# Optimization experiments

Measured on AMD Instinct MI355X. Metric: run time of the kernel, lower is better.

The kernel has to match this reference:

```python
import jax, jax.numpy as jnp
import numpy as np

B, S, H, Q, K = 16, 4096, 1024, 1024, 2048


def setup_inputs() -> dict:
    key = jax.random.key(0)
    k0, k1, k2, k3, k4, k5 = jax.random.split(key, 6)
    return {
        "mask": jax.random.randint(k0, (B, 1, S), 0, 2, dtype=jnp.int32),
        "query": jax.random.normal(k1, (B, 1, Q), dtype=jnp.float32),
        "proj_key": jax.random.normal(k2, (B, S, H), dtype=jnp.float32),
        "value": jax.random.normal(k3, (B, S, K), dtype=jnp.float32),
        "Wq": jax.random.normal(k4, (H, Q), dtype=jnp.float32) * 0.02,
        "w_energy": jax.random.normal(k5, (H,), dtype=jnp.float32) * 0.02,
    }


def reference(mask, query, proj_key, value, Wq, w_energy):
    # query_layer: [B,1,Q] @ Wq^T -> [B,1,H]
    q = jnp.einsum("btq,hq->bth", query, Wq)
    # energy_layer(tanh(q + proj_key)): broadcast add over seq, dot with w_energy -> [B,S]
    scores = jnp.einsum("bsh,h->bs", jnp.tanh(q + proj_key), w_energy)
    scores = scores[:, None, :]  # [B,1,S]
    scores = jnp.where(mask == 0, -jnp.inf, scores)
    alphas = jax.nn.softmax(scores, axis=-1)  # [B,1,S]
    context = jnp.einsum("bts,bsk->btk", alphas, value)  # [B,1,K]
    return (context, alphas)
```

## Files before the change

### kernel.cpp

```cpp
#include <hip/hip_runtime.h>
#include <math.h>

#define B_ 16
#define S_ 4096
#define H_ 1024
#define Q_ 1024
#define K_ 2048

__device__ __forceinline__ float fast_tanh(float x) {
    float e = __expf(2.0f * x);
    float r = __builtin_amdgcn_rcpf(e + 1.0f);
    return 1.0f - 2.0f * r;
}

__device__ __forceinline__ float wave_reduce_sum(float v) {
#pragma unroll
    for (int off = 32; off > 0; off >>= 1)
        v += __shfl_xor(v, off, 64);
    return v;
}

__global__ __launch_bounds__(256) void qproj_kernel(const float* __restrict__ query,
                                                    const float* __restrict__ Wq,
                                                    float* __restrict__ qws) {
    int wave = (blockIdx.x * 256 + threadIdx.x) >> 6;
    int lane = threadIdx.x & 63;
    int b = wave >> 10;
    int h = wave & 1023;
    const float4* wrow = (const float4*)(Wq + (size_t)h * Q_);
    const float4* qrow = (const float4*)(query + (size_t)b * Q_);
    float acc = 0.f;
#pragma unroll
    for (int m = 0; m < 4; ++m) {
        int i = m * 64 + lane;
        float4 w = wrow[i];
        float4 q = qrow[i];
        acc += w.x * q.x + w.y * q.y + w.z * q.z + w.w * q.w;
    }
    acc = wave_reduce_sum(acc);
    if (lane == 0) qws[wave] = acc;
}

__global__ __launch_bounds__(256) void scores_kernel(const float* __restrict__ pk,
                                                     const float* __restrict__ qws,
                                                     const float* __restrict__ we,
                                                     float* __restrict__ scores) {
    int row  = (blockIdx.x * 256 + threadIdx.x) >> 6;
    int lane = threadIdx.x & 63;
    int b = row >> 12;
    const float4* prow = (const float4*)(pk + (size_t)row * H_);
    const float4* qrow = (const float4*)(qws + (size_t)b * H_);
    const float4* wrow = (const float4*)we;
    float acc = 0.f;
#pragma unroll
    for (int m = 0; m < 4; ++m) {
        int i = m * 64 + lane;
        float4 p = prow[i];
        float4 q = qrow[i];
        float4 w = wrow[i];
        acc += fast_tanh(q.x + p.x) * w.x;
        acc += fast_tanh(q.y + p.y) * w.y;
        acc += fast_tanh(q.z + p.z) * w.z;
        acc += fast_tanh(q.w + p.w) * w.w;
    }
    acc = wave_reduce_sum(acc);
    if (lane == 0) scores[row] = acc;
}

__global__ __launch_bounds__(256) void softmax_kernel(const float* __restrict__ scores,
                                                      const int* __restrict__ mask,
                                                      float* __restrict__ alphas) {
    int b = blockIdx.x;
    int tid = threadIdx.x;
    __shared__ float red[8];
    float v[16];
    float lmax = -INFINITY;
#pragma unroll
    for (int m = 0; m < 16; ++m) {
        int s = m * 256 + tid;
        float sc = scores[b * S_ + s];
        int mk = mask[b * S_ + s];
        v[m] = mk ? sc : -INFINITY;
        lmax = fmaxf(lmax, v[m]);
    }
#pragma unroll
    for (int off = 32; off > 0; off >>= 1)
        lmax = fmaxf(lmax, __shfl_xor(lmax, off, 64));
    int wid = tid >> 6;
    if ((tid & 63) == 0) red[wid] = lmax;
    __syncthreads();
    float mx = fmaxf(fmaxf(red[0], red[1]), fmaxf(red[2], red[3]));
    float lsum = 0.f;
#pragma unroll
    for (int m = 0; m < 16; ++m) {
        float e = (v[m] == -INFINITY) ? 0.f : __expf(v[m] - mx);
        v[m] = e;
        lsum += e;
    }
    lsum = wave_reduce_sum(lsum);
    if ((tid & 63) == 0) red[4 + wid] = lsum;
    __syncthreads();
    float total = red[4] + red[5] + red[6] + red[7];
    float rinv = 1.0f / total;
#pragma unroll
    for (int m = 0; m < 16; ++m) {
        int s = m * 256 + tid;
        alphas[b * S_ + s] = v[m] * rinv;
    }
}

__global__ __launch_bounds__(256) void context_partial_kernel(const float* __restrict__ value,
                                                              const float* __restrict__ alphas,
                                                              float* __restrict__ partial,
                                                              int schunks, int L) {
    extern __shared__ float la[];
    int c  = blockIdx.x;
    int kt = blockIdx.y;
    int b  = blockIdx.z;
    int tid = threadIdx.x;
    int s0 = c * L;
    for (int i = tid; i < L; i += 256) la[i] = alphas[b * S_ + s0 + i];
    __syncthreads();
    const float4* vp = (const float4*)(value + ((size_t)(b * S_ + s0)) * K_ + kt * 1024) + tid;
    float4 acc = make_float4(0.f, 0.f, 0.f, 0.f);
#pragma unroll 4
    for (int i = 0; i < L; ++i) {
        float a = la[i];
        float4 vv = vp[(size_t)i * (K_ / 4)];
        acc.x = fmaf(a, vv.x, acc.x);
        acc.y = fmaf(a, vv.y, acc.y);
        acc.z = fmaf(a, vv.z, acc.z);
        acc.w = fmaf(a, vv.w, acc.w);
    }
    float4* pout = (float4*)(partial + ((size_t)(b * schunks + c)) * K_ + kt * 1024) + tid;
    *pout = acc;
}

__global__ __launch_bounds__(256) void context_reduce_kernel(const float* __restrict__ partial,
                                                             float* __restrict__ ctx,
                                                             int schunks) {
    int idx = blockIdx.x * 256 + threadIdx.x;
    int b = idx >> 11;
    int k = idx & 2047;
    float acc = 0.f;
    for (int c = 0; c < schunks; ++c)
        acc += partial[((size_t)(b * schunks + c)) * K_ + k];
    ctx[idx] = acc;
}

extern "C" void kernel_launch(void* const* d_in, const int* in_sizes, int n_in,
                              void* d_out, int out_size, void* d_ws, size_t ws_size,
                              hipStream_t stream) {
    const int*   mask     = (const int*)d_in[0];
    const float* query    = (const float*)d_in[1];
    const float* proj_key = (const float*)d_in[2];
    const float* value    = (const float*)d_in[3];
    const float* Wq       = (const float*)d_in[4];
    const float* w_energy = (const float*)d_in[5];

    float* out    = (float*)d_out;
    float* ctx    = out;
    float* alphas = out + B_ * K_;

    float* ws      = (float*)d_ws;
    float* qws     = ws;
    float* scores  = ws + B_ * H_;
    float* partial = ws + B_ * H_ + B_ * S_;

    size_t avail = ws_size / 4;
    size_t head  = (size_t)B_ * H_ + (size_t)B_ * S_;
    avail = (avail > head) ? (avail - head) : 0;
    int schunks = 32;
    while (schunks > 1 && (size_t)schunks * B_ * K_ > avail) schunks >>= 1;
    int L = S_ / schunks;

    qproj_kernel<<<(B_ * H_) / 4, 256, 0, stream>>>(query, Wq, qws);
    scores_kernel<<<(B_ * S_) / 4, 256, 0, stream>>>(proj_key, qws, w_energy, scores);
    softmax_kernel<<<B_, 256, 0, stream>>>(scores, mask, alphas);
    dim3 g4(schunks, K_ / 1024, B_);
    context_partial_kernel<<<g4, 256, (size_t)L * sizeof(float), stream>>>(value, alphas, partial,
                                                                           schunks, L);
    context_reduce_kernel<<<(B_ * K_) / 256, 256, 0, stream>>>(partial, ctx, schunks);
}
```

Measured before the change: 833.5 us.

## Skip masked positions in scores and gather only unmasked value rows

Scores kernel exits early for masked rows, avoiding proj_key reads and tanh work for them. Softmax now builds a compacted list of unmasked indices and their alphas via a block prefix scan, and the context kernel iterates only over those entries, gathering value rows by index. This cuts memory traffic roughly in proportion to the masked fraction, at the cost of an extra scan and indirect row addressing.

After: 785.8 us. -5.7%, faster.

```diff
diff --git a/kernel.cpp b/kernel.cpp
--- a/kernel.cpp
+++ b/kernel.cpp
@@ -44,9 +44,11 @@
 __global__ __launch_bounds__(256) void scores_kernel(const float* __restrict__ pk,
                                                      const float* __restrict__ qws,
                                                      const float* __restrict__ we,
+                                                     const int* __restrict__ mask,
                                                      float* __restrict__ scores) {
     int row  = (blockIdx.x * 256 + threadIdx.x) >> 6;
     int lane = threadIdx.x & 63;
+    if (mask[row] == 0) return;
     int b = row >> 12;
     const float4* prow = (const float4*)(pk + (size_t)row * H_);
     const float4* qrow = (const float4*)(qws + (size_t)b * H_);
@@ -69,19 +71,27 @@
 
 __global__ __launch_bounds__(256) void softmax_kernel(const float* __restrict__ scores,
                                                       const int* __restrict__ mask,
-                                                      float* __restrict__ alphas) {
+                                                      float* __restrict__ alphas,
+                                                      int* __restrict__ cidx,
+                                                      float* __restrict__ calpha,
+                                                      int* __restrict__ count) {
     int b = blockIdx.x;
     int tid = threadIdx.x;
     __shared__ float red[8];
+    __shared__ int scan[256];
     float v[16];
+    int mk[16];
+    int base = b * S_ + tid * 16;
     float lmax = -INFINITY;
+    int myc = 0;
 #pragma unroll
     for (int m = 0; m < 16; ++m) {
-        int s = m * 256 + tid;
-        float sc = scores[b * S_ + s];
-        int mk = mask[b * S_ + s];
-        v[m] = mk ? sc : -INFINITY;
+        float sc = scores[base + m];
+        int mm = mask[base + m];
+        mk[m] = mm;
+        v[m] = mm ? sc : -INFINITY;
         lmax = fmaxf(lmax, v[m]);
+        myc += (mm != 0);
     }
 #pragma unroll
     for (int off = 32; off > 0; off >>= 1)
@@ -93,7 +103,7 @@
     float lsum = 0.f;
 #pragma unroll
     for (int m = 0; m < 16; ++m) {
-        float e = (v[m] == -INFINITY) ? 0.f : __expf(v[m] - mx);
+        float e = mk[m] ? __expf(v[m] - mx) : 0.f;
         v[m] = e;
         lsum += e;
     }
@@ -102,31 +112,58 @@
     __syncthreads();
     float total = red[4] + red[5] + red[6] + red[7];
     float rinv = 1.0f / total;
+    scan[tid] = myc;
+    __syncthreads();
+    for (int off = 1; off < 256; off <<= 1) {
+        int t = (tid >= off) ? scan[tid - off] : 0;
+        __syncthreads();
+        scan[tid] += t;
+        __syncthreads();
+    }
+    int pos = scan[tid] - myc;
+    if (tid == 255) count[b] = scan[255];
 #pragma unroll
     for (int m = 0; m < 16; ++m) {
-        int s = m * 256 + tid;
-        alphas[b * S_ + s] = v[m] * rinv;
+        float a = v[m] * rinv;
+        alphas[base + m] = a;
+        if (mk[m]) {
+            cidx[b * S_ + pos]   = tid * 16 + m;
+            calpha[b * S_ + pos] = a;
+            pos++;
+        }
     }
 }
 
 __global__ __launch_bounds__(256) void context_partial_kernel(const float* __restrict__ value,
-                                                              const float* __restrict__ alphas,
+                                                              const float* __restrict__ calpha,
+                                                              const int* __restrict__ cidx,
+                                                              const int* __restrict__ count,
                                                               float* __restrict__ partial,
-                                                              int schunks, int L) {
-    extern __shared__ float la[];
+                                                              int schunks, int Lmax) {
+    extern __shared__ float sh[];
+    float* la = sh;
+    int*   li = (int*)(sh + Lmax);
     int c  = blockIdx.x;
     int kt = blockIdx.y;
     int b  = blockIdx.z;
     int tid = threadIdx.x;
-    int s0 = c * L;
-    for (int i = tid; i < L; i += 256) la[i] = alphas[b * S_ + s0 + i];
-    __syncthreads();
-    const float4* vp = (const float4*)(value + ((size_t)(b * S_ + s0)) * K_ + kt * 1024) + tid;
+    int cnt = count[b];
+    int L = (cnt + schunks - 1) / schunks;
+    int j0 = c * L;
+    int j1 = j0 + L; if (j1 > cnt) j1 = cnt;
+    int n = j1 - j0; if (n < 0) n = 0;
+    for (int i = tid; i < n; i += 256) {
+        la[i] = calpha[b * S_ + j0 + i];
+        li[i] = cidx[b * S_ + j0 + i];
+    }
+    __syncthreads();
+    const float* vbase = value + (size_t)b * S_ * K_ + kt * 1024;
     float4 acc = make_float4(0.f, 0.f, 0.f, 0.f);
 #pragma unroll 4
-    for (int i = 0; i < L; ++i) {
+    for (int i = 0; i < n; ++i) {
         float a = la[i];
-        float4 vv = vp[(size_t)i * (K_ / 4)];
+        int   s = li[i];
+        float4 vv = *((const float4*)(vbase + (size_t)s * K_) + tid);
         acc.x = fmaf(a, vv.x, acc.x);
         acc.y = fmaf(a, vv.y, acc.y);
         acc.z = fmaf(a, vv.z, acc.z);
@@ -164,21 +201,25 @@
 
     float* ws      = (float*)d_ws;
     float* qws     = ws;
-    float* scores  = ws + B_ * H_;
-    float* partial = ws + B_ * H_ + B_ * S_;
-
+    float* scores  = qws + B_ * H_;
+    float* calpha  = scores + B_ * S_;
+    int*   cidx    = (int*)(calpha + B_ * S_);
+    int*   count   = cidx + B_ * S_;
+    float* partial = (float*)(count + 64);
+
+    size_t used_head = (size_t)(B_ * H_ + 3 * B_ * S_ + 64);
     size_t avail = ws_size / 4;
-    size_t head  = (size_t)B_ * H_ + (size_t)B_ * S_;
-    avail = (avail > head) ? (avail - head) : 0;
+    avail = (avail > used_head) ? (avail - used_head) : 0;
     int schunks = 32;
     while (schunks > 1 && (size_t)schunks * B_ * K_ > avail) schunks >>= 1;
-    int L = S_ / schunks;
+    int Lmax = (S_ + schunks - 1) / schunks;
 
     qproj_kernel<<<(B_ * H_) / 4, 256, 0, stream>>>(query, Wq, qws);
-    scores_kernel<<<(B_ * S_) / 4, 256, 0, stream>>>(proj_key, qws, w_energy, scores);
-    softmax_kernel<<<B_, 256, 0, stream>>>(scores, mask, alphas);
+    scores_kernel<<<(B_ * S_) / 4, 256, 0, stream>>>(proj_key, qws, w_energy, mask, scores);
+    softmax_kernel<<<B_, 256, 0, stream>>>(scores, mask, alphas, cidx, calpha, count);
     dim3 g4(schunks, K_ / 1024, B_);
-    context_partial_kernel<<<g4, 256, (size_t)L * sizeof(float), stream>>>(value, alphas, partial,
-                                                                           schunks, L);
+    size_t shbytes = (size_t)Lmax * (sizeof(float) + sizeof(int));
+    context_partial_kernel<<<g4, 256, shbytes, stream>>>(value, calpha, cidx, count, partial,
+                                                         schunks, Lmax);
     context_reduce_kernel<<<(B_ * K_) / 256, 256, 0, stream>>>(partial, ctx, schunks);
 }
```
